# Performance work log

Hardware: AMD Instinct MI355X
Metric: run time of the kernel (lower is better)

## Reference

```python
import jax, jax.numpy as jnp
import numpy as np

N_NODES = 100000
N_EDGES = 1600000
HEADS = 2
D_HEAD = 64


def _transformer_conv(x, src, dst, Wq, bq, Wk, bk, Wv, bv, Ws, bs):
    # PyG TransformerConv (concat=True, beta=False, root_weight=True)
    N = x.shape[0]
    H, D = HEADS, D_HEAD
    q = (x @ Wq + bq).reshape(N, H, D)
    k = (x @ Wk + bk).reshape(N, H, D)
    v = (x @ Wv + bv).reshape(N, H, D)
    scale = np.float32(1.0 / np.sqrt(D))
    # per-edge attention logits [E, H]; messages flow src -> dst
    logits = (q[dst] * k[src]).sum(-1) * scale
    m = jax.ops.segment_max(logits, dst, num_segments=N)  # [N, H]
    e = jnp.exp(logits - m[dst])                          # [E, H]
    denom = jax.ops.segment_sum(e, dst, num_segments=N)   # [N, H]
    num = jax.ops.segment_sum(e[:, :, None] * v[src], dst, num_segments=N)  # [N, H, D]
    out = num / jnp.maximum(denom, 1e-16)[:, :, None]
    return out.reshape(N, H * D) + (x @ Ws + bs)


def setup_inputs() -> dict:
    key = jax.random.key(0)
    ks = jax.random.split(key, 16)
    d = {}
    d['x'] = jax.random.normal(ks[0], (N_NODES, 128), dtype=jnp.float32)
    d['edge_index'] = jax.random.randint(ks[1], (2, N_EDGES), 0, N_NODES, dtype=jnp.int64)
    s = 0.05
    d['Wq1'] = jax.random.normal(ks[2], (128, 128), jnp.float32) * s
    d['bq1'] = jnp.zeros((128,), jnp.float32)
    d['Wk1'] = jax.random.normal(ks[3], (128, 128), jnp.float32) * s
    d['bk1'] = jnp.zeros((128,), jnp.float32)
    d['Wv1'] = jax.random.normal(ks[4], (128, 128), jnp.float32) * s
    d['bv1'] = jnp.zeros((128,), jnp.float32)
    d['Ws1'] = jax.random.normal(ks[5], (128, 128), jnp.float32) * s
    d['bs1'] = jnp.zeros((128,), jnp.float32)
    d['Wq2'] = jax.random.normal(ks[6], (128, 128), jnp.float32) * s
    d['bq2'] = jnp.zeros((128,), jnp.float32)
    d['Wk2'] = jax.random.normal(ks[7], (128, 128), jnp.float32) * s
    d['bk2'] = jnp.zeros((128,), jnp.float32)
    d['Wv2'] = jax.random.normal(ks[8], (128, 128), jnp.float32) * s
    d['bv2'] = jnp.zeros((128,), jnp.float32)
    d['Ws2'] = jax.random.normal(ks[9], (128, 128), jnp.float32) * s
    d['bs2'] = jnp.zeros((128,), jnp.float32)
    d['Wc'] = jax.random.normal(ks[10], (128, 40), jnp.float32) * s
    d['bc'] = jnp.zeros((40,), jnp.float32)
    return d


def reference(x, edge_index, Wq1, bq1, Wk1, bk1, Wv1, bv1, Ws1, bs1,
              Wq2, bq2, Wk2, bk2, Wv2, bv2, Ws2, bs2, Wc, bc):
    src, dst = edge_index[0], edge_index[1]
    h = _transformer_conv(x, src, dst, Wq1, bq1, Wk1, bk1, Wv1, bv1, Ws1, bs1)
    h = jax.nn.elu(h)  # dropout is eval-mode no-op
    h = _transformer_conv(h, src, dst, Wq2, bq2, Wk2, bk2, Wv2, bv2, Ws2, bs2)
    return h @ Wc + bc
```

## Files before the change

### kernel.cpp

```cpp
#include <hip/hip_runtime.h>
#include <hip/hip_bf16.h>
#include <math.h>

#define FDIM 128

typedef unsigned int uint;
typedef unsigned short ushort;
typedef __attribute__((ext_vector_type(8))) short short8;
typedef __attribute__((ext_vector_type(4))) float f32x4;
typedef __attribute__((ext_vector_type(2))) uint uintv2;
typedef __attribute__((ext_vector_type(4))) uint uintv4;
typedef __attribute__((ext_vector_type(4))) float floatv4;
typedef __attribute__((ext_vector_type(2))) int intv2;

__device__ inline ushort f2bf(float f) {
  uint u = __float_as_uint(f);
  uint r = (u + 0x7fffu + ((u >> 16) & 1u)) >> 16;
  return (ushort)r;
}
#define BFLO(u) __uint_as_float(((uint)(u)) << 16)
#define BFHI(u) __uint_as_float((u) & 0xffff0000u)

__device__ inline float dot2bf(uint a, uint b, float c) {
  float d;
  asm("v_dot2_f32_bf16 %0, %1, %2, %3" : "=v"(d) : "v"(a), "v"(b), "v"(c));
  return d;
}


__global__ __launch_bounds__(256) void k_hist(const int* __restrict__ ei, int E,
                                              int* __restrict__ cnt) {
  const int* dsts = ei + E;
  int base = blockIdx.x * 4096 + threadIdx.x;
#pragma unroll
  for (int i = 0; i < 16; ++i) {
    int e = base + i * 256;
    if (e < E) atomicAdd(&cnt[dsts[e]], 1);
  }
}

__global__ __launch_bounds__(256) void k_scatter(const int* __restrict__ ei, int E,
                                                 int* __restrict__ cur,
                                                 int* __restrict__ ssrc) {
  const int* dsts = ei + E;
  int base = blockIdx.x * 4096 + threadIdx.x;
#pragma unroll
  for (int i = 0; i < 16; ++i) {
    int e = base + i * 256;
    if (e < E) {
      int pos = atomicAdd(&cur[dsts[e]], 1);
      ssrc[pos] = ei[e] << 9;
    }
  }
}

__global__ __launch_bounds__(256) void k_scan1(const int* __restrict__ cnt,
                                               int* __restrict__ loc,
                                               int* __restrict__ bsum, int N) {
  __shared__ int ws[4];
  int tid = threadIdx.x, lane = tid & 63, wid = tid >> 6;
  int i = blockIdx.x * 1024 + tid * 4;
  int4 v = {0, 0, 0, 0};
  if (i + 3 < N) v = *(const int4*)&cnt[i];
  else {
    if (i < N) v.x = cnt[i];
    if (i + 1 < N) v.y = cnt[i + 1];
    if (i + 2 < N) v.z = cnt[i + 2];
    if (i + 3 < N) v.w = cnt[i + 3];
  }
  int s0 = v.x, s1 = s0 + v.y, s2 = s1 + v.z, s3 = s2 + v.w;
  int x = s3;
#pragma unroll
  for (int d = 1; d < 64; d <<= 1) {
    int y = __shfl_up(x, d, 64);
    if (lane >= d) x += y;
  }
  if (lane == 63) ws[wid] = x;
  __syncthreads();
  int woff = 0;
  for (int k = 0; k < wid; ++k) woff += ws[k];
  int excl = woff + (x - s3);
  if (i < N) loc[i] = excl;
  if (i + 1 < N) loc[i + 1] = excl + s0;
  if (i + 2 < N) loc[i + 2] = excl + s1;
  if (i + 3 < N) loc[i + 3] = excl + s2;
  if (tid == 255) bsum[blockIdx.x] = woff + x;
}

__global__ __launch_bounds__(256) void k_scan2(int* __restrict__ bsum, int nb) {
  __shared__ int ws[4];
  __shared__ int ctot;
  int tid = threadIdx.x, lane = tid & 63, wid = tid >> 6;
  int carry = 0;
  for (int base = 0; base < nb; base += 256) {
    int i = base + tid;
    int v = (i < nb) ? bsum[i] : 0;
    int x = v;
#pragma unroll
    for (int d = 1; d < 64; d <<= 1) {
      int y = __shfl_up(x, d, 64);
      if (lane >= d) x += y;
    }
    if (lane == 63) ws[wid] = x;
    __syncthreads();
    if (tid == 0) {
      int run = 0;
#pragma unroll
      for (int k = 0; k < 4; ++k) { int t = ws[k]; ws[k] = run; run += t; }
      ctot = run;
    }
    __syncthreads();
    if (i < nb) bsum[i] = carry + ws[wid] + (x - v);
    carry += ctot;
    __syncthreads();
  }
}

__global__ __launch_bounds__(256) void k_scan3(const int* __restrict__ loc,
                                               const int* __restrict__ bsum,
                                               intv2* __restrict__ begend,
                                               int* __restrict__ cur,
                                               int N, int E) {
  int i = blockIdx.x * blockDim.x + threadIdx.x;
  if (i < N) {
    int v = loc[i] + bsum[i >> 10];
    int vn = (i + 1 < N) ? (loc[i + 1] + bsum[(i + 1) >> 10]) : E;
    intv2 be; be.x = v; be.y = vn;
    begend[i] = be;
    cur[i] = v;
  }
}


__global__ __launch_bounds__(256) void k_cvtw(
    const float* __restrict__ Wq1, const float* __restrict__ Wk1,
    const float* __restrict__ Wv1, const float* __restrict__ Ws1,
    const float* __restrict__ Wq2, const float* __restrict__ Wk2,
    const float* __restrict__ Wv2, const float* __restrict__ Ws2,
    ushort* __restrict__ Wt1, ushort* __restrict__ Wt2) {
  int idx = blockIdx.x * 256 + threadIdx.x;
  int which = idx >> 16;
  int m = (idx >> 14) & 3;
  int e = idx & 16383;
  int n = e >> 7, k = e & 127;
  const float* W;
  if (which == 0) W = (m == 0) ? Wq1 : (m == 1) ? Wk1 : (m == 2) ? Wv1 : Ws1;
  else            W = (m == 0) ? Wq2 : (m == 1) ? Wk2 : (m == 2) ? Wv2 : Ws2;
  ushort* o = which ? Wt2 : Wt1;
  o[(size_t)(m * 128 + n) * 128 + k] = f2bf(W[k * 128 + n]);
}

__global__ __launch_bounds__(256) void k_cvtwc(const float* __restrict__ Wc,
                                               ushort* __restrict__ Wct) {
  int j = blockIdx.x * 256 + threadIdx.x;
  if (j >= 48 * 128) return;
  int n = j >> 7, k = j & 127;
  float w = (n < 40) ? Wc[k * 40 + n] : 0.f;
  ushort hi = f2bf(w);
  float res = w - BFLO(hi);
  Wct[j] = hi;
  Wct[48 * 128 + j] = f2bf(res);
}


#define LPAD 136

__global__ __launch_bounds__(256) void k_gemm_qkvs(
    const void* __restrict__ Araw, int aF32, const ushort* __restrict__ Wt,
    const float* __restrict__ bq, const float* __restrict__ bk,
    const float* __restrict__ bv, const float* __restrict__ bs,
    ushort* __restrict__ qb, ushort* __restrict__ kvb, ushort* __restrict__ skb,
    int N) {
  __shared__ ushort sA[128 * LPAD];
  __shared__ ushort sB[128 * LPAD];
  int tid = threadIdx.x;
  int bm = blockIdx.x * 128;

  for (int c = tid; c < 128 * 16; c += 256) {
    int r = c >> 4, kc = (c & 15) * 8;
    int gr = bm + r;
    uint4 val = {0, 0, 0, 0};
    if (gr < N) {
      if (aF32) {
        const float* xr = (const float*)Araw + (size_t)gr * 128 + kc;
        floatv4 f0 = *(const floatv4*)xr;
        floatv4 f1 = *(const floatv4*)(xr + 4);
        val.x = (uint)f2bf(f0.x) | ((uint)f2bf(f0.y) << 16);
        val.y = (uint)f2bf(f0.z) | ((uint)f2bf(f0.w) << 16);
        val.z = (uint)f2bf(f1.x) | ((uint)f2bf(f1.y) << 16);
        val.w = (uint)f2bf(f1.z) | ((uint)f2bf(f1.w) << 16);
      } else {
        val = *(const uint4*)((const ushort*)Araw + (size_t)gr * 128 + kc);
      }
    }
    *(uint4*)&sA[r * LPAD + kc] = val;
  }

  int lane = tid & 63, wv = tid >> 6;
  int ml = lane & 15, quad = lane >> 4;
  const ushort* pA0 = &sA[(32 * wv + ml) * LPAD + quad * 8];
  const ushort* pA1 = &sA[(32 * wv + 16 + ml) * LPAD + quad * 8];
  const ushort* pB = &sB[ml * LPAD + quad * 8];

#pragma unroll
  for (int mat = 0; mat < 4; ++mat) {
    __syncthreads();
    for (int c = tid; c < 128 * 16; c += 256) {
      int r = c >> 4, kc = (c & 15) * 8;
      uint4 val = *(const uint4*)&Wt[(size_t)(mat * 128 + r) * 128 + kc];
      *(uint4*)&sB[r * LPAD + kc] = val;
    }
    __syncthreads();

    f32x4 acc0[8] = {}, acc1[8] = {};
#pragma unroll
    for (int k0 = 0; k0 < 128; k0 += 32) {
      short8 a0 = *(const short8*)&pA0[k0];
      short8 a1 = *(const short8*)&pA1[k0];
#pragma unroll
      for (int ct = 0; ct < 8; ++ct) {
        short8 b = *(const short8*)&pB[ct * 16 * LPAD + k0];
        acc0[ct] = __builtin_amdgcn_mfma_f32_16x16x32_bf16(a0, b, acc0[ct], 0, 0, 0);
        acc1[ct] = __builtin_amdgcn_mfma_f32_16x16x32_bf16(a1, b, acc1[ct], 0, 0, 0);
      }
    }
    __syncthreads();

    const float* B = (mat == 0) ? bq : (mat == 1) ? bk : (mat == 2) ? bv : bs;
    float oscale = (mat == 0) ? 0.1803368801f : 1.0f;
    int r0 = 32 * wv + quad * 4;
#pragma unroll
    for (int ct = 0; ct < 8; ++ct) {
      int c = ct * 16 + ml;
      float bias = B[c];
#pragma unroll
      for (int r = 0; r < 4; ++r) {
        sB[(r0 + r) * LPAD + c] = f2bf((acc0[ct][r] + bias) * oscale);
        sB[(r0 + 16 + r) * LPAD + c] = f2bf((acc1[ct][r] + bias) * oscale);
      }
    }
    __syncthreads();

    ushort* obase = (mat == 0) ? qb : (mat == 3) ? skb : kvb;
    int ostride = (mat == 1 || mat == 2) ? 256 : 128;
    int ooff = (mat == 2) ? 128 : 0;
    for (int c = tid; c < 128 * 16; c += 256) {
      int r = c >> 4, kc = (c & 15) * 8;
      int gr = bm + r;
      if (gr < N) {
        uintv4 val = *(const uintv4*)&sB[r * LPAD + kc];
        __builtin_nontemporal_store(
            val, (uintv4*)&obase[(size_t)gr * ostride + ooff + kc]);
      }
    }
  }
}


__global__ __launch_bounds__(256) void k_attn(const ushort* __restrict__ qb,
                                              const ushort* __restrict__ kvb,
                                              const ushort* __restrict__ skb,
                                              const intv2* __restrict__ begend,
                                              const int* __restrict__ ssrc,
                                              ushort* __restrict__ outb,
                                              int N, int applyElu) {
  int n = (int)(blockIdx.x * (blockDim.x >> 6)) + (threadIdx.x >> 6);
  int lane = threadIdx.x & 63;
  if (n >= N) return;
  int g = lane >> 4;
  int hl = lane & 15;
  int dim0 = hl * 8;
  int hB = hl << 4;
  const char* kvB = (const char*)kvb;
  uintv4 qu = __builtin_nontemporal_load((const uintv4*)&qb[(size_t)n * FDIM + dim0]);
  intv2 be = __builtin_nontemporal_load(&begend[n]);
  int beg = be.x, end = be.y;
  float lsum = 0.f;
  float a0 = 0.f, a1 = 0.f, a2 = 0.f, a3 = 0.f;
  float a4 = 0.f, a5 = 0.f, a6 = 0.f, a7 = 0.f;

#define QKDOT(ku_) dot2bf(ku_.w, qu.w, dot2bf(ku_.z, qu.z,                     \
                    dot2bf(ku_.y, qu.y, dot2bf(ku_.x, qu.x, 0.f))))
#define ACCV(pe_, vu_)                                                         \
  lsum += pe_;                                                                 \
  a0 += pe_ * BFLO(vu_.x); a1 += pe_ * BFHI(vu_.x);                            \
  a2 += pe_ * BFLO(vu_.y); a3 += pe_ * BFHI(vu_.y);                            \
  a4 += pe_ * BFLO(vu_.z); a5 += pe_ * BFHI(vu_.z);                            \
  a6 += pe_ * BFLO(vu_.w); a7 += pe_ * BFHI(vu_.w);

#define EDGE1(T)                                                               \
  {                                                                            \
    int t_ = (T);                                                              \
    int s_ = __shfl(slane, t_, 64);                                            \
    const ushort* p_ = (const ushort*)(kvB + (uint)s_ + hB);                   \
    uintv4 ku_ = *(const uintv4*)p_;                                           \
    uintv4 vu_ = *(const uintv4*)(p_ + 128);                                   \
    float d_ = QKDOT(ku_);                                                     \
    d_ += __shfl_xor(d_, 1, 64);                                               \
    d_ += __shfl_xor(d_, 2, 64);                                               \
    d_ += __shfl_xor(d_, 4, 64);                                               \
    float p_e = (t_ < cnt) ? __builtin_exp2f(d_) : 0.f;                        \
    ACCV(p_e, vu_);                                                            \
  }

  for (int j0 = beg; j0 < end; j0 += 64) {
    int cnt = end - j0; if (cnt > 64) cnt = 64;
    int slane = (j0 + lane < end)
                    ? __builtin_nontemporal_load(&ssrc[j0 + lane]) : 0;
    int nIter = (cnt + 3) >> 2;
    int it = 0;
    for (; it + 3 <= nIter; it += 3) {
      int t0 = g + 4 * it;
      int s0 = __shfl(slane, t0, 64);
      int s1 = __shfl(slane, t0 + 4, 64);
      int s2 = __shfl(slane, t0 + 8, 64);
      const ushort* p0 = (const ushort*)(kvB + (uint)s0 + hB);
      const ushort* p1 = (const ushort*)(kvB + (uint)s1 + hB);
      const ushort* p2 = (const ushort*)(kvB + (uint)s2 + hB);
      uintv4 k0 = *(const uintv4*)p0, v0 = *(const uintv4*)(p0 + 128);
      uintv4 k1 = *(const uintv4*)p1, v1 = *(const uintv4*)(p1 + 128);
      uintv4 k2 = *(const uintv4*)p2, v2 = *(const uintv4*)(p2 + 128);
      float d0 = QKDOT(k0), d1 = QKDOT(k1), d2 = QKDOT(k2);
      d0 += __shfl_xor(d0, 1, 64); d1 += __shfl_xor(d1, 1, 64);
      d2 += __shfl_xor(d2, 1, 64);
      d0 += __shfl_xor(d0, 2, 64); d1 += __shfl_xor(d1, 2, 64);
      d2 += __shfl_xor(d2, 2, 64);
      d0 += __shfl_xor(d0, 4, 64); d1 += __shfl_xor(d1, 4, 64);
      d2 += __shfl_xor(d2, 4, 64);
      float e0 = (t0     < cnt) ? __builtin_exp2f(d0) : 0.f;
      float e1 = (t0 + 4 < cnt) ? __builtin_exp2f(d1) : 0.f;
      float e2 = (t0 + 8 < cnt) ? __builtin_exp2f(d2) : 0.f;
      ACCV(e0, v0); ACCV(e1, v1); ACCV(e2, v2);
    }
    for (; it < nIter; ++it) {
      EDGE1(g + 4 * it);
    }
  }
#undef EDGE1
#undef ACCV
#undef QKDOT

  lsum += __shfl_xor(lsum, 16, 64);
  a0 += __shfl_xor(a0, 16, 64); a1 += __shfl_xor(a1, 16, 64);
  a2 += __shfl_xor(a2, 16, 64); a3 += __shfl_xor(a3, 16, 64);
  a4 += __shfl_xor(a4, 16, 64); a5 += __shfl_xor(a5, 16, 64);
  a6 += __shfl_xor(a6, 16, 64); a7 += __shfl_xor(a7, 16, 64);
  lsum += __shfl_xor(lsum, 32, 64);
  a0 += __shfl_xor(a0, 32, 64); a1 += __shfl_xor(a1, 32, 64);
  a2 += __shfl_xor(a2, 32, 64); a3 += __shfl_xor(a3, 32, 64);
  a4 += __shfl_xor(a4, 32, 64); a5 += __shfl_xor(a5, 32, 64);
  a6 += __shfl_xor(a6, 32, 64); a7 += __shfl_xor(a7, 32, 64);
  float inv = 1.f / fmaxf(lsum, 1e-16f);
  if (g == 0) {
    uintv4 su = __builtin_nontemporal_load((const uintv4*)&skb[(size_t)n * FDIM + dim0]);
    float r0 = a0 * inv + BFLO(su.x);
    float r1 = a1 * inv + BFHI(su.x);
    float r2 = a2 * inv + BFLO(su.y);
    float r3 = a3 * inv + BFHI(su.y);
    float r4 = a4 * inv + BFLO(su.z);
    float r5 = a5 * inv + BFHI(su.z);
    float r6 = a6 * inv + BFLO(su.w);
    float r7 = a7 * inv + BFHI(su.w);
    if (applyElu) {
      r0 = (r0 > 0.f) ? r0 : (__expf(r0) - 1.f);
      r1 = (r1 > 0.f) ? r1 : (__expf(r1) - 1.f);
      r2 = (r2 > 0.f) ? r2 : (__expf(r2) - 1.f);
      r3 = (r3 > 0.f) ? r3 : (__expf(r3) - 1.f);
      r4 = (r4 > 0.f) ? r4 : (__expf(r4) - 1.f);
      r5 = (r5 > 0.f) ? r5 : (__expf(r5) - 1.f);
      r6 = (r6 > 0.f) ? r6 : (__expf(r6) - 1.f);
      r7 = (r7 > 0.f) ? r7 : (__expf(r7) - 1.f);
    }
    uintv4 p;
    p.x = (uint)f2bf(r0) | ((uint)f2bf(r1) << 16);
    p.y = (uint)f2bf(r2) | ((uint)f2bf(r3) << 16);
    p.z = (uint)f2bf(r4) | ((uint)f2bf(r5) << 16);
    p.w = (uint)f2bf(r6) | ((uint)f2bf(r7) << 16);
    __builtin_nontemporal_store(p, (uintv4*)&outb[(size_t)n * FDIM + dim0]);
  }
}


__global__ __launch_bounds__(256) void k_final(const ushort* __restrict__ H,
                                               const ushort* __restrict__ Wct,
                                               const float* __restrict__ bc,
                                               float* __restrict__ out, int N) {
  __shared__ ushort sH[128 * LPAD];
  __shared__ ushort sW[96 * LPAD];
  int tid = threadIdx.x;
  int bm = blockIdx.x * 128;

  for (int c = tid; c < 128 * 16; c += 256) {
    int r = c >> 4, kc = (c & 15) * 8;
    int gr = bm + r;
    uint4 val = {0, 0, 0, 0};
    if (gr < N) val = *(const uint4*)&H[(size_t)gr * 128 + kc];
    *(uint4*)&sH[r * LPAD + kc] = val;
  }
  for (int c = tid; c < 96 * 16; c += 256) {
    int r = c >> 4, kc = (c & 15) * 8;
    uint4 val = *(const uint4*)&Wct[(size_t)r * 128 + kc];
    *(uint4*)&sW[r * LPAD + kc] = val;
  }
  __syncthreads();

  int lane = tid & 63, wv = tid >> 6;
  int ml = lane & 15, quad = lane >> 4;
  const ushort* pA0 = &sH[(32 * wv + ml) * LPAD + quad * 8];
  const ushort* pA1 = &sH[(32 * wv + 16 + ml) * LPAD + quad * 8];
  const ushort* pBh = &sW[ml * LPAD + quad * 8];
  const ushort* pBl = &sW[(48 + ml) * LPAD + quad * 8];
  f32x4 acc0[3] = {}, acc1[3] = {};
#pragma unroll
  for (int k0 = 0; k0 < 128; k0 += 32) {
    short8 a0 = *(const short8*)&pA0[k0];
    short8 a1 = *(const short8*)&pA1[k0];
#pragma unroll
    for (int ct = 0; ct < 3; ++ct) {
      short8 bh = *(const short8*)&pBh[ct * 16 * LPAD + k0];
      short8 bl = *(const short8*)&pBl[ct * 16 * LPAD + k0];
      acc0[ct] = __builtin_amdgcn_mfma_f32_16x16x32_bf16(a0, bh, acc0[ct], 0, 0, 0);
      acc0[ct] = __builtin_amdgcn_mfma_f32_16x16x32_bf16(a0, bl, acc0[ct], 0, 0, 0);
      acc1[ct] = __builtin_amdgcn_mfma_f32_16x16x32_bf16(a1, bh, acc1[ct], 0, 0, 0);
      acc1[ct] = __builtin_amdgcn_mfma_f32_16x16x32_bf16(a1, bl, acc1[ct], 0, 0, 0);
    }
  }
  __syncthreads();

  float* sO = (float*)sH;
  int r0 = 32 * wv + quad * 4;
#pragma unroll
  for (int ct = 0; ct < 3; ++ct) {
    int c = ct * 16 + ml;
    float bias = (c < 40) ? bc[c] : 0.f;
#pragma unroll
    for (int r = 0; r < 4; ++r) {
      sO[(r0 + r) * 48 + c] = acc0[ct][r] + bias;
      sO[(r0 + 16 + r) * 48 + c] = acc1[ct][r] + bias;
    }
  }
  __syncthreads();

  for (int i = tid; i < 128 * 10; i += 256) {
    int r = i / 10, seg = i % 10;
    int gr = bm + r;
    if (gr < N) {
      floatv4 v = *(const floatv4*)&sO[r * 48 + seg * 4];
      __builtin_nontemporal_store(v, (floatv4*)&out[(size_t)gr * 40 + seg * 4]);
    }
  }
}


#define ALIGN_UP(p) ((char*)(((size_t)(p) + 255) & ~(size_t)255))

extern "C" void kernel_launch(void* const* d_in, const int* in_sizes, int n_in,
                              void* d_out, int out_size, void* d_ws, size_t ws_size,
                              hipStream_t stream) {
  const float* x  = (const float*)d_in[0];
  const int*   ei = (const int*)d_in[1];
  const float* Wq1 = (const float*)d_in[2],  *bq1 = (const float*)d_in[3];
  const float* Wk1 = (const float*)d_in[4],  *bk1 = (const float*)d_in[5];
  const float* Wv1 = (const float*)d_in[6],  *bv1 = (const float*)d_in[7];
  const float* Ws1 = (const float*)d_in[8],  *bs1 = (const float*)d_in[9];
  const float* Wq2 = (const float*)d_in[10], *bq2 = (const float*)d_in[11];
  const float* Wk2 = (const float*)d_in[12], *bk2 = (const float*)d_in[13];
  const float* Wv2 = (const float*)d_in[14], *bv2 = (const float*)d_in[15];
  const float* Ws2 = (const float*)d_in[16], *bs2 = (const float*)d_in[17];
  const float* Wc  = (const float*)d_in[18], *bc  = (const float*)d_in[19];

  int N = in_sizes[0] / FDIM;
  int E = in_sizes[1] / 2;

  char* w = (char*)d_ws;
  ushort* qb  = (ushort*)w; w = ALIGN_UP(w + (size_t)N * 128 * sizeof(ushort));
  ushort* kvb = (ushort*)w; w = ALIGN_UP(w + (size_t)N * 256 * sizeof(ushort));
  ushort* skb = (ushort*)w; w = ALIGN_UP(w + (size_t)N * 128 * sizeof(ushort));
  ushort* ab16 = (ushort*)w; w = ALIGN_UP(w + (size_t)N * 128 * sizeof(ushort));
  ushort* Wt1 = (ushort*)w; w = ALIGN_UP(w + (size_t)512 * 128 * sizeof(ushort));
  ushort* Wt2 = (ushort*)w; w = ALIGN_UP(w + (size_t)512 * 128 * sizeof(ushort));
  ushort* Wct = (ushort*)w; w = ALIGN_UP(w + (size_t)2 * 48 * 128 * sizeof(ushort));
  intv2* begend = (intv2*)w; w = ALIGN_UP(w + (size_t)N * sizeof(intv2));
  int* cnt  = (int*)w;      w = ALIGN_UP(w + (size_t)N * sizeof(int));
  int* loc  = (int*)w;      w = ALIGN_UP(w + (size_t)N * sizeof(int));
  int* bsum = (int*)w;      w = ALIGN_UP(w + 1024 * sizeof(int));
  int* ssrc = (int*)w;

  int nb = (N + 1023) / 1024;
  int eb = (E + 4095) / 4096;

  hipMemsetAsync(cnt, 0, (size_t)N * sizeof(int), stream);
  k_hist<<<eb, 256, 0, stream>>>(ei, E, cnt);
  k_scan1<<<nb, 256, 0, stream>>>(cnt, loc, bsum, N);
  k_scan2<<<1, 256, 0, stream>>>(bsum, nb);
  k_scan3<<<(N + 255) / 256, 256, 0, stream>>>(loc, bsum, begend, cnt, N, E);
  k_scatter<<<eb, 256, 0, stream>>>(ei, E, cnt, ssrc);

  k_cvtw<<<512, 256, 0, stream>>>(Wq1, Wk1, Wv1, Ws1, Wq2, Wk2, Wv2, Ws2, Wt1, Wt2);
  k_cvtwc<<<24, 256, 0, stream>>>(Wc, Wct);

  int gblocks = (N + 127) / 128;
  int ablocks = (N + 3) / 4;

  k_gemm_qkvs<<<gblocks, 256, 0, stream>>>(x, 1, Wt1, bq1, bk1, bv1, bs1, qb, kvb, skb, N);
  k_attn<<<ablocks, 256, 0, stream>>>(qb, kvb, skb, begend, ssrc, ab16, N, 1);

  k_gemm_qkvs<<<gblocks, 256, 0, stream>>>(ab16, 0, Wt2, bq2, bk2, bv2, bs2, qb, kvb, skb, N);
  k_attn<<<ablocks, 256, 0, stream>>>(qb, kvb, skb, begend, ssrc, ab16, N, 0);

  k_final<<<gblocks, 256, 0, stream>>>(ab16, Wct, bc, (float*)d_out, N);
}
```

Measured before the change: 655.3 us.

## Partition CSR histogram and scatter atomics by destination range across eight block groups

The edge histogram and scatter kernels now launch eight times as many blocks. Each block handles only edges whose destination falls in one eighth of the node range, chosen by blockIdx mod 8. Since consecutive blocks are spread round-robin over the chip's dies, each die's atomics should stay on a compact slice of the counter array, which is meant to improve cache locality and cut atomic traffic between dies. In exchange, the destination array is read eight times, and seven of every eight loaded edges are discarded.

```diff
diff --git a/kernel.cpp b/kernel.cpp
--- a/kernel.cpp
+++ b/kernel.cpp
@@ -28,28 +28,42 @@
 }
 
 
-__global__ __launch_bounds__(256) void k_hist(const int* __restrict__ ei, int E,
-                                              int* __restrict__ cnt) {
+__global__ __launch_bounds__(256) void k_hist8(const int* __restrict__ ei, int E,
+                                               int N, int* __restrict__ cnt) {
+  int part = blockIdx.x & 7;
+  int chunk = blockIdx.x >> 3;
+  int lo = (int)(((long long)part * N) >> 3);
+  int hi = (int)(((long long)(part + 1) * N) >> 3);
   const int* dsts = ei + E;
-  int base = blockIdx.x * 4096 + threadIdx.x;
-#pragma unroll
-  for (int i = 0; i < 16; ++i) {
-    int e = base + i * 256;
-    if (e < E) atomicAdd(&cnt[dsts[e]], 1);
-  }
-}
-
-__global__ __launch_bounds__(256) void k_scatter(const int* __restrict__ ei, int E,
-                                                 int* __restrict__ cur,
-                                                 int* __restrict__ ssrc) {
-  const int* dsts = ei + E;
-  int base = blockIdx.x * 4096 + threadIdx.x;
+  int base = chunk * 4096 + threadIdx.x;
 #pragma unroll
   for (int i = 0; i < 16; ++i) {
     int e = base + i * 256;
     if (e < E) {
-      int pos = atomicAdd(&cur[dsts[e]], 1);
-      ssrc[pos] = ei[e] << 9;
+      int d = dsts[e];
+      if (d >= lo && d < hi) atomicAdd(&cnt[d], 1);
+    }
+  }
+}
+
+__global__ __launch_bounds__(256) void k_scatter8(const int* __restrict__ ei, int E,
+                                                  int N, int* __restrict__ cur,
+                                                  int* __restrict__ ssrc) {
+  int part = blockIdx.x & 7;
+  int chunk = blockIdx.x >> 3;
+  int lo = (int)(((long long)part * N) >> 3);
+  int hi = (int)(((long long)(part + 1) * N) >> 3);
+  const int* dsts = ei + E;
+  int base = chunk * 4096 + threadIdx.x;
+#pragma unroll
+  for (int i = 0; i < 16; ++i) {
+    int e = base + i * 256;
+    if (e < E) {
+      int d = dsts[e];
+      if (d >= lo && d < hi) {
+        int pos = atomicAdd(&cur[d], 1);
+        ssrc[pos] = ei[e] << 9;
+      }
     }
   }
 }
@@ -487,14 +501,14 @@
   int* ssrc = (int*)w;
 
   int nb = (N + 1023) / 1024;
-  int eb = (E + 4095) / 4096;
+  int C8 = 8 * ((E + 4095) / 4096);
 
   hipMemsetAsync(cnt, 0, (size_t)N * sizeof(int), stream);
-  k_hist<<<eb, 256, 0, stream>>>(ei, E, cnt);
+  k_hist8<<<C8, 256, 0, stream>>>(ei, E, N, cnt);
   k_scan1<<<nb, 256, 0, stream>>>(cnt, loc, bsum, N);
   k_scan2<<<1, 256, 0, stream>>>(bsum, nb);
   k_scan3<<<(N + 255) / 256, 256, 0, stream>>>(loc, bsum, begend, cnt, N, E);
-  k_scatter<<<eb, 256, 0, stream>>>(ei, E, cnt, ssrc);
+  k_scatter8<<<C8, 256, 0, stream>>>(ei, E, N, cnt, ssrc);
 
   k_cvtw<<<512, 256, 0, stream>>>(Wq1, Wk1, Wv1, Ws1, Wq2, Wk2, Wv2, Ws2, Wt1, Wt2);
   k_cvtwc<<<24, 256, 0, stream>>>(Wc, Wct);
```

After: 613.4 us. -6.4%, faster.
